# Kernel optimization log

Hardware: AMD Instinct MI355X
Metric: run time of the kernel (lower is better)

## Reference

```python
import jax, jax.numpy as jnp
import numpy as np

B = 64            # number of graphs
NPG = 64          # nodes per graph (static; lengths are all equal here)
N = B * NPG       # total nodes = sum(lengths)
LT = 128          # max text tokens per node
LL = 32           # max labels per node
VOCAB = 50000
TOTAL_NUM = 100000
D = 256           # embedding_text == embedding_label == hidden_dimension
OUT = 1024


def setup_inputs() -> dict:
    key = jax.random.key(0)
    ks = jax.random.split(key, 12)
    return {
        "text_ids": jax.random.randint(ks[0], (N, LT), 0, VOCAB),
        "label_ids": jax.random.randint(ks[1], (N, LL), 0, TOTAL_NUM),
        "text_len": jax.random.randint(ks[2], (N,), 1, LT + 1),
        "label_len": jax.random.randint(ks[3], (N,), 1, LL + 1),
        "word_emb": jax.random.normal(ks[4], (VOCAB, D), jnp.float32) * 0.02,
        "label_emb": jax.random.normal(ks[5], (TOTAL_NUM, D), jnp.float32) * 0.02,
        "Wg_text": jax.random.normal(ks[6], (D, D), jnp.float32) * (1.0 / np.sqrt(D)),
        "Wg_label": jax.random.normal(ks[7], (D, D), jnp.float32) * (1.0 / np.sqrt(D)),
        "w_adap": jax.random.normal(ks[8], (2,), jnp.float32),
        "W1": jax.random.normal(ks[9], (D, D), jnp.float32) * (1.0 / np.sqrt(D)),
        "b1": jnp.zeros((D,), jnp.float32),
        "Wout": jax.random.normal(ks[10], (D, OUT), jnp.float32) * (1.0 / np.sqrt(D)),
        "bout": jnp.zeros((OUT,), jnp.float32),
    }


def _ragged_bag(table, ids, lens, mean):
    # gather rows then masked sum over the ragged axis (EmbeddingBag-style)
    L = ids.shape[1]
    mask = (jnp.arange(L)[None, :] < lens[:, None]).astype(table.dtype)  # [N, L]
    emb = table[ids]                                                     # [N, L, D]
    out = jnp.einsum("nld,nl->nd", emb, mask)
    if mean:
        out = out / lens[:, None].astype(table.dtype)
    return out


def reference(text_ids, label_ids, text_len, label_len, word_emb, label_emb,
              Wg_text, Wg_label, w_adap, W1, b1, Wout, bout):
    # fetchFeature: per-node ragged mean of word embeddings, ragged sum of label embeddings
    text_out = _ragged_bag(word_emb, text_ids, text_len, mean=True)    # [N, D]
    label_out = _ragged_bag(label_emb, label_ids, label_len, mean=False)  # [N, D]

    # weighted_GCN surrogate: per-type linear projection + relu, then per-graph mean readout
    h_t = jax.nn.relu(text_out @ Wg_text)   # [N, D]
    h_l = jax.nn.relu(label_out @ Wg_label)  # [N, D]
    seg = jnp.repeat(jnp.arange(B), NPG)     # graph id per node
    r_t = jax.ops.segment_sum(h_t, seg, num_segments=B) / NPG  # [B, D]
    r_l = jax.ops.segment_sum(h_l, seg, num_segments=B) / NPG  # [B, D]

    # adap: Linear(2,1,bias=False) over stacked (text,label), then MLLinear fusion
    fused = jnp.stack([r_t, r_l], axis=-1) @ w_adap  # [B, D]
    h = jax.nn.relu(fused @ W1 + b1)
    return h @ Wout + bout  # [B, OUT]
```

## Files before the change

### kernel.cpp

```cpp
#include <hip/hip_runtime.h>

#define NN      4096
#define BG      64
#define NPG_    64
#define LT_     128
#define LL_     32
#define D_      256
#define OUT_    1024

typedef __attribute__((ext_vector_type(8))) short bf16x8;
typedef __attribute__((ext_vector_type(4))) float f32x4;

__device__ __forceinline__ void split_bf16(float v, unsigned short& hi, unsigned short& lo) {
    union { float f; unsigned u; } a; a.f = v;
    const unsigned hu = (a.u + 0x8000u) & 0xFFFF0000u;
    union { unsigned u; float f; } h; h.u = hu;
    const float r = v - h.f;
    union { float f; unsigned u; } b; b.f = r;
    hi = (unsigned short)(hu >> 16);
    lo = (unsigned short)(((b.u + 0x8000u) & 0xFFFF0000u) >> 16);
}

__global__ __launch_bounds__(256) void gather_kernel(
    const int*   __restrict__ text_ids,
    const int*   __restrict__ label_ids,
    const int*   __restrict__ text_len,
    const int*   __restrict__ label_len,
    const float* __restrict__ word_emb,
    const float* __restrict__ label_emb,
    const float* __restrict__ Wg_text,
    const float* __restrict__ Wg_label,
    unsigned short* __restrict__ Wpk,
    unsigned short* __restrict__ xh_t,
    unsigned short* __restrict__ xl_t,
    unsigned short* __restrict__ xh_l,
    unsigned short* __restrict__ xl_l)
{
    const int tid  = threadIdx.x;

    if (blockIdx.x >= NN) {
        const int b   = blockIdx.x - NN;
        const int mat = b >> 7;
        const int nt  = (b >> 3) & 15;
        const int ks  = b & 7;
        const float* __restrict__ W = mat ? Wg_label : Wg_text;
        #pragma unroll
        for (int r = 0; r < 2; ++r) {
            const int idx = tid + 256 * r;
            const int kl  = idx >> 4;
            const int c16 = idx & 15;
            const int k   = ks * 32 + kl;
            const float v = W[(size_t)k * D_ + nt * 16 + c16];
            unsigned short h, l;
            split_bf16(v, h, l);
            const int lane = c16 + 16 * ((kl >> 3) & 3);
            const int e    = kl & 7;
            const size_t pb = (((size_t)nt * 8 + ks) * 4 + mat * 2) * 512 + lane * 8 + e;
            Wpk[pb]       = h;
            Wpk[pb + 512] = l;
        }
        return;
    }

    __shared__ int   sIds[LT_ + LL_];
    __shared__ float redT[4][D_];
    __shared__ float redL[4][D_];

    const int n    = blockIdx.x;
    const int wave = tid >> 6;
    const int lane = tid & 63;

    if (tid < LT_)               sIds[tid] = text_ids [(size_t)n * LT_ + tid];
    else if (tid < LT_ + LL_)    sIds[tid] = label_ids[(size_t)n * LL_ + (tid - LT_)];
    const int lt = text_len[n];
    const int ll = label_len[n];
    __syncthreads();

    float4 aT = make_float4(0.f, 0.f, 0.f, 0.f);
    float4 aL = make_float4(0.f, 0.f, 0.f, 0.f);

    {
        const float* __restrict__ bp = word_emb + (size_t)lane * 4;
        #pragma unroll 8
        for (int l = wave; l < lt; l += 4) {
            const float4 v = *reinterpret_cast<const float4*>(bp + (size_t)sIds[l] * D_);
            aT.x += v.x; aT.y += v.y; aT.z += v.z; aT.w += v.w;
        }
    }
    {
        const float* __restrict__ bp = label_emb + (size_t)lane * 4;
        #pragma unroll 8
        for (int l = wave; l < ll; l += 4) {
            const float4 v = *reinterpret_cast<const float4*>(bp + (size_t)sIds[LT_ + l] * D_);
            aL.x += v.x; aL.y += v.y; aL.z += v.z; aL.w += v.w;
        }
    }

    *reinterpret_cast<float4*>(&redT[wave][lane * 4]) = aT;
    *reinterpret_cast<float4*>(&redL[wave][lane * 4]) = aL;
    __syncthreads();

    const float t  = ((redT[0][tid] + redT[1][tid]) + (redT[2][tid] + redT[3][tid])) / (float)lt;
    const float lv =  (redL[0][tid] + redL[1][tid]) + (redL[2][tid] + redL[3][tid]);

    unsigned short h, l;
    const size_t o = (size_t)n * D_ + tid;
    split_bf16(t,  h, l);  xh_t[o] = h;  xl_t[o] = l;
    split_bf16(lv, h, l);  xh_l[o] = h;  xl_l[o] = l;
}

__global__ __launch_bounds__(256, 4) void proj_kernel(
    const unsigned short* __restrict__ xh_t,
    const unsigned short* __restrict__ xl_t,
    const unsigned short* __restrict__ xh_l,
    const unsigned short* __restrict__ xl_l,
    const unsigned short* __restrict__ Wpk,
    const float* __restrict__ w_adap,
    float*       __restrict__ h_comb)
{
    __shared__ __align__(16) short ldsX[4][16 * D_];

    const int tid   = threadIdx.x;
    const int wave  = tid >> 6;
    const int lane  = tid & 63;
    const int ntile = blockIdx.x >> 2;
    const int cq    = blockIdx.x & 3;
    const int base  = ntile * 16;

    #pragma unroll
    for (int r = 0; r < 2; ++r) {
        const int idx = tid + 256 * r;
        const int nd  = idx >> 5, ch = idx & 31;
        const size_t g = (size_t)(base + nd) * D_ + ch * 8;
        const int d = nd * D_ + ((ch ^ (nd & 7)) * 8);
        *reinterpret_cast<int4*>(&ldsX[0][d]) = *reinterpret_cast<const int4*>(&xh_t[g]);
        *reinterpret_cast<int4*>(&ldsX[1][d]) = *reinterpret_cast<const int4*>(&xl_t[g]);
        *reinterpret_cast<int4*>(&ldsX[2][d]) = *reinterpret_cast<const int4*>(&xh_l[g]);
        *reinterpret_cast<int4*>(&ldsX[3][d]) = *reinterpret_cast<const int4*>(&xl_l[g]);
    }
    __syncthreads();

    const int nt  = cq * 4 + wave;
    const int row = lane & 15;
    const int kc  = lane >> 4;
    const unsigned short* __restrict__ WpB = Wpk + ((size_t)nt * 8) * 4 * 512 + lane * 8;

    f32x4 accT = {0.f, 0.f, 0.f, 0.f};
    f32x4 accL = {0.f, 0.f, 0.f, 0.f};

    bf16x8 cA0, cA1, cA2, cA3, cB0, cB1, cB2, cB3;
    bf16x8 nA0, nA1, nA2, nA3, nB0, nB1, nB2, nB3;

    {
        const int aidx = row * D_ + ((kc ^ (row & 7)) * 8);
        cA0 = *reinterpret_cast<const bf16x8*>(&ldsX[0][aidx]);
        cA1 = *reinterpret_cast<const bf16x8*>(&ldsX[1][aidx]);
        cA2 = *reinterpret_cast<const bf16x8*>(&ldsX[2][aidx]);
        cA3 = *reinterpret_cast<const bf16x8*>(&ldsX[3][aidx]);
        const unsigned short* p = WpB;
        cB0 = *reinterpret_cast<const bf16x8*>(p);
        cB1 = *reinterpret_cast<const bf16x8*>(p + 512);
        cB2 = *reinterpret_cast<const bf16x8*>(p + 1024);
        cB3 = *reinterpret_cast<const bf16x8*>(p + 1536);
    }

    #pragma unroll
    for (int ks = 0; ks < 8; ++ks) {
        if (ks < 7) {
            const int aidx = row * D_ + ((((ks + 1) * 4 + kc) ^ (row & 7)) * 8);
            nA0 = *reinterpret_cast<const bf16x8*>(&ldsX[0][aidx]);
            nA1 = *reinterpret_cast<const bf16x8*>(&ldsX[1][aidx]);
            nA2 = *reinterpret_cast<const bf16x8*>(&ldsX[2][aidx]);
            nA3 = *reinterpret_cast<const bf16x8*>(&ldsX[3][aidx]);
            const unsigned short* p = WpB + (size_t)(ks + 1) * 2048;
            nB0 = *reinterpret_cast<const bf16x8*>(p);
            nB1 = *reinterpret_cast<const bf16x8*>(p + 512);
            nB2 = *reinterpret_cast<const bf16x8*>(p + 1024);
            nB3 = *reinterpret_cast<const bf16x8*>(p + 1536);
        }

        accT = __builtin_amdgcn_mfma_f32_16x16x32_bf16(cA0, cB0, accT, 0, 0, 0);
        accT = __builtin_amdgcn_mfma_f32_16x16x32_bf16(cA0, cB1, accT, 0, 0, 0);
        accT = __builtin_amdgcn_mfma_f32_16x16x32_bf16(cA1, cB0, accT, 0, 0, 0);
        accL = __builtin_amdgcn_mfma_f32_16x16x32_bf16(cA2, cB2, accL, 0, 0, 0);
        accL = __builtin_amdgcn_mfma_f32_16x16x32_bf16(cA2, cB3, accL, 0, 0, 0);
        accL = __builtin_amdgcn_mfma_f32_16x16x32_bf16(cA3, cB2, accL, 0, 0, 0);

        cA0 = nA0; cA1 = nA1; cA2 = nA2; cA3 = nA3;
        cB0 = nB0; cB1 = nB1; cB2 = nB2; cB3 = nB3;
    }

    const float w0r = w_adap[0] * (1.0f / (float)NPG_);
    const float w1r = w_adap[1] * (1.0f / (float)NPG_);
    #pragma unroll
    for (int r = 0; r < 4; ++r) {
        const int node = base + kc * 4 + r;
        const int col  = nt * 16 + row;
        const float ht = accT[r] > 0.f ? accT[r] : 0.f;
        const float hl = accL[r] > 0.f ? accL[r] : 0.f;
        h_comb[(size_t)node * D_ + col] = w0r * ht + w1r * hl;
    }
}

__global__ __launch_bounds__(256) void graph_kernel(
    const float* __restrict__ h_comb,
    const float* __restrict__ W1,
    const float* __restrict__ b1,
    const float* __restrict__ Wout,
    const float* __restrict__ bout,
    float*       __restrict__ out)
{
    __shared__ float fused[D_];
    __shared__ float hrow[D_];

    const int bx   = blockIdx.x;
    const int b    = bx >> 2;
    const int part = bx & 3;
    const int tid  = threadIdx.x;

    float acc = 0.f;
    const float* __restrict__ basep = h_comb + (size_t)b * NPG_ * D_ + tid;
    #pragma unroll 8
    for (int n = 0; n < NPG_; ++n) acc += basep[(size_t)n * D_];
    fused[tid] = acc;
    __syncthreads();

    {
        float s0 = 0.f, s1 = 0.f, s2 = 0.f, s3 = 0.f;
        const float* __restrict__ wp = W1 + tid;
        for (int d = 0; d < D_; d += 4) {
            s0 = fmaf(fused[d + 0], wp[(size_t)(d + 0) * D_], s0);
            s1 = fmaf(fused[d + 1], wp[(size_t)(d + 1) * D_], s1);
            s2 = fmaf(fused[d + 2], wp[(size_t)(d + 2) * D_], s2);
            s3 = fmaf(fused[d + 3], wp[(size_t)(d + 3) * D_], s3);
        }
        const float a1 = b1[tid] + ((s0 + s1) + (s2 + s3));
        hrow[tid] = a1 > 0.f ? a1 : 0.f;
    }
    __syncthreads();

    const int j = part * 256 + tid;
    {
        float s0 = 0.f, s1 = 0.f, s2 = 0.f, s3 = 0.f;
        const float* __restrict__ wp = Wout + j;
        for (int d = 0; d < D_; d += 4) {
            s0 = fmaf(hrow[d + 0], wp[(size_t)(d + 0) * OUT_], s0);
            s1 = fmaf(hrow[d + 1], wp[(size_t)(d + 1) * OUT_], s1);
            s2 = fmaf(hrow[d + 2], wp[(size_t)(d + 2) * OUT_], s2);
            s3 = fmaf(hrow[d + 3], wp[(size_t)(d + 3) * OUT_], s3);
        }
        out[(size_t)b * OUT_ + j] = bout[j] + ((s0 + s1) + (s2 + s3));
    }
}

extern "C" void kernel_launch(void* const* d_in, const int* in_sizes, int n_in,
                              void* d_out, int out_size, void* d_ws, size_t ws_size,
                              hipStream_t stream) {
    const int*   text_ids  = (const int*)  d_in[0];
    const int*   label_ids = (const int*)  d_in[1];
    const int*   text_len  = (const int*)  d_in[2];
    const int*   label_len = (const int*)  d_in[3];
    const float* word_emb  = (const float*)d_in[4];
    const float* label_emb = (const float*)d_in[5];
    const float* Wg_text   = (const float*)d_in[6];
    const float* Wg_label  = (const float*)d_in[7];
    const float* w_adap    = (const float*)d_in[8];
    const float* W1        = (const float*)d_in[9];
    const float* b1        = (const float*)d_in[10];
    const float* Wout      = (const float*)d_in[11];
    const float* bout      = (const float*)d_in[12];

    char* ws = (char*)d_ws;
    float*          h_comb = (float*)ws;
    unsigned short* xh_t   = (unsigned short*)(ws + (4  << 20));
    unsigned short* xl_t   = (unsigned short*)(ws + (6  << 20));
    unsigned short* xh_l   = (unsigned short*)(ws + (8  << 20));
    unsigned short* xl_l   = (unsigned short*)(ws + (10 << 20));
    unsigned short* Wpk    = (unsigned short*)(ws + (12 << 20));
    float*          out    = (float*)d_out;

    gather_kernel<<<NN + 256, 256, 0, stream>>>(
        text_ids, label_ids, text_len, label_len,
        word_emb, label_emb, Wg_text, Wg_label, Wpk,
        xh_t, xl_t, xh_l, xl_l);

    proj_kernel<<<NN / 16 * 4, 256, 0, stream>>>(
        xh_t, xl_t, xh_l, xl_l, Wpk, w_adap, h_comb);

    graph_kernel<<<BG * 4, 256, 0, stream>>>(
        h_comb, W1, b1, Wout, bout, out);
}
```

Baseline: 84.70 us.

## Convert word table to bf16 each call and drop split-bf16 activation precision

Adds a prep kernel that converts the whole 50000x256 fp32 word embedding table to bf16 on every call, and gathers text rows from that half-size table. The gathered activations are now stored as single bf16 instead of a hi/lo split, which halves the workspace traffic and cuts the MFMA count in the projection from six to four per k-step. The cost is a full-table conversion pass (about 51MB read and 26MB written) on every call, plus lower precision in the activations and the embedding values.

```diff
diff --git a/kernel.cpp b/kernel.cpp
--- a/kernel.cpp
+++ b/kernel.cpp
@@ -7,10 +7,20 @@
 #define LL_     32
 #define D_      256
 #define OUT_    1024
+#define VOCAB_  50000
 
 typedef __attribute__((ext_vector_type(8))) short bf16x8;
 typedef __attribute__((ext_vector_type(4))) float f32x4;
 
+__device__ __forceinline__ unsigned short f2bf_rne(float f) {
+    union { float f; unsigned u; } a; a.f = f;
+    const unsigned r = a.u + 0x7FFFu + ((a.u >> 16) & 1u);
+    return (unsigned short)(r >> 16);
+}
+__device__ __forceinline__ float bf2f(unsigned short h) {
+    union { unsigned u; float f; } a; a.u = ((unsigned)h) << 16;
+    return a.f;
+}
 __device__ __forceinline__ void split_bf16(float v, unsigned short& hi, unsigned short& lo) {
     union { float f; unsigned u; } a; a.f = v;
     const unsigned hu = (a.u + 0x8000u) & 0xFFFF0000u;
@@ -21,52 +31,66 @@
     lo = (unsigned short)(((b.u + 0x8000u) & 0xFFFF0000u) >> 16);
 }
 
+__global__ __launch_bounds__(256) void prep_kernel(
+    const float* __restrict__ word_emb,
+    const float* __restrict__ Wg_text,
+    const float* __restrict__ Wg_label,
+    const int convBlocks,
+    unsigned short* __restrict__ wtab,
+    unsigned short* __restrict__ Wpk)
+{
+    const int tid = threadIdx.x;
+    if (blockIdx.x < convBlocks) {
+        const int total4 = VOCAB_ * D_ / 4;
+        const int stride = convBlocks * 256;
+        for (int i = blockIdx.x * 256 + tid; i < total4; i += stride) {
+            const float4 v = *reinterpret_cast<const float4*>(word_emb + (size_t)i * 4);
+            ushort4 o;
+            o.x = f2bf_rne(v.x); o.y = f2bf_rne(v.y);
+            o.z = f2bf_rne(v.z); o.w = f2bf_rne(v.w);
+            *reinterpret_cast<ushort4*>(wtab + (size_t)i * 4) = o;
+        }
+        return;
+    }
+    const int b   = blockIdx.x - convBlocks;
+    const int mat = b >> 7;
+    const int nt  = (b >> 3) & 15;
+    const int ks  = b & 7;
+    const float* __restrict__ W = mat ? Wg_label : Wg_text;
+    #pragma unroll
+    for (int r = 0; r < 2; ++r) {
+        const int idx = tid + 256 * r;
+        const int kl  = idx >> 4;
+        const int c16 = idx & 15;
+        const int k   = ks * 32 + kl;
+        const float v = W[(size_t)k * D_ + nt * 16 + c16];
+        unsigned short h, l;
+        split_bf16(v, h, l);
+        const int lane = c16 + 16 * ((kl >> 3) & 3);
+        const int e    = kl & 7;
+        const size_t pb = (((size_t)nt * 8 + ks) * 4 + mat * 2) * 512 + lane * 8 + e;
+        Wpk[pb]       = h;
+        Wpk[pb + 512] = l;
+    }
+}
+
+template<bool BF16TAB>
 __global__ __launch_bounds__(256) void gather_kernel(
     const int*   __restrict__ text_ids,
     const int*   __restrict__ label_ids,
     const int*   __restrict__ text_len,
     const int*   __restrict__ label_len,
     const float* __restrict__ word_emb,
+    const unsigned short* __restrict__ wtab,
     const float* __restrict__ label_emb,
-    const float* __restrict__ Wg_text,
-    const float* __restrict__ Wg_label,
-    unsigned short* __restrict__ Wpk,
-    unsigned short* __restrict__ xh_t,
-    unsigned short* __restrict__ xl_t,
-    unsigned short* __restrict__ xh_l,
-    unsigned short* __restrict__ xl_l)
+    unsigned short* __restrict__ xb_t,
+    unsigned short* __restrict__ xb_l)
 {
+    __shared__ int   sIds[LT_ + LL_];
+    __shared__ float red[8][D_];
+
+    const int n    = blockIdx.x;
     const int tid  = threadIdx.x;
-
-    if (blockIdx.x >= NN) {
-        const int b   = blockIdx.x - NN;
-        const int mat = b >> 7;
-        const int nt  = (b >> 3) & 15;
-        const int ks  = b & 7;
-        const float* __restrict__ W = mat ? Wg_label : Wg_text;
-        #pragma unroll
-        for (int r = 0; r < 2; ++r) {
-            const int idx = tid + 256 * r;
-            const int kl  = idx >> 4;
-            const int c16 = idx & 15;
-            const int k   = ks * 32 + kl;
-            const float v = W[(size_t)k * D_ + nt * 16 + c16];
-            unsigned short h, l;
-            split_bf16(v, h, l);
-            const int lane = c16 + 16 * ((kl >> 3) & 3);
-            const int e    = kl & 7;
-            const size_t pb = (((size_t)nt * 8 + ks) * 4 + mat * 2) * 512 + lane * 8 + e;
-            Wpk[pb]       = h;
-            Wpk[pb + 512] = l;
-        }
-        return;
-    }
-
-    __shared__ int   sIds[LT_ + LL_];
-    __shared__ float redT[4][D_];
-    __shared__ float redL[4][D_];
-
-    const int n    = blockIdx.x;
     const int wave = tid >> 6;
     const int lane = tid & 63;
 
@@ -76,17 +100,31 @@
     const int ll = label_len[n];
     __syncthreads();
 
-    float4 aT = make_float4(0.f, 0.f, 0.f, 0.f);
-    float4 aL = make_float4(0.f, 0.f, 0.f, 0.f);
-
-    {
+    float ta[8];
+    float4 aT4 = make_float4(0.f, 0.f, 0.f, 0.f);
+    if (BF16TAB) {
+        #pragma unroll
+        for (int j = 0; j < 8; ++j) ta[j] = 0.f;
+        const int h  = lane >> 5;
+        const int cg = lane & 31;
+        const int s  = wave * 2 + h;
+        const unsigned short* __restrict__ bp = wtab + cg * 8;
+        #pragma unroll 4
+        for (int l = s; l < lt; l += 8) {
+            const bf16x8 v = *reinterpret_cast<const bf16x8*>(bp + (size_t)sIds[l] * D_);
+            #pragma unroll
+            for (int j = 0; j < 8; ++j) ta[j] += bf2f((unsigned short)v[j]);
+        }
+    } else {
         const float* __restrict__ bp = word_emb + (size_t)lane * 4;
         #pragma unroll 8
         for (int l = wave; l < lt; l += 4) {
             const float4 v = *reinterpret_cast<const float4*>(bp + (size_t)sIds[l] * D_);
-            aT.x += v.x; aT.y += v.y; aT.z += v.z; aT.w += v.w;
-        }
-    }
+            aT4.x += v.x; aT4.y += v.y; aT4.z += v.z; aT4.w += v.w;
+        }
+    }
+
+    float4 aL = make_float4(0.f, 0.f, 0.f, 0.f);
     {
         const float* __restrict__ bp = label_emb + (size_t)lane * 4;
         #pragma unroll 8
@@ -96,29 +134,39 @@
         }
     }
 
-    *reinterpret_cast<float4*>(&redT[wave][lane * 4]) = aT;
-    *reinterpret_cast<float4*>(&redL[wave][lane * 4]) = aL;
-    __syncthreads();
-
-    const float t  = ((redT[0][tid] + redT[1][tid]) + (redT[2][tid] + redT[3][tid])) / (float)lt;
-    const float lv =  (redL[0][tid] + redL[1][tid]) + (redL[2][tid] + redL[3][tid]);
-
-    unsigned short h, l;
+    if (BF16TAB) {
+        const int h = lane >> 5, cg = lane & 31, s = wave * 2 + h;
+        *reinterpret_cast<float4*>(&red[s][cg * 8])     = make_float4(ta[0], ta[1], ta[2], ta[3]);
+        *reinterpret_cast<float4*>(&red[s][cg * 8 + 4]) = make_float4(ta[4], ta[5], ta[6], ta[7]);
+    } else {
+        *reinterpret_cast<float4*>(&red[wave][lane * 4]) = aT4;
+    }
+    __syncthreads();
+    float t;
+    if (BF16TAB)
+        t = ((red[0][tid] + red[1][tid]) + (red[2][tid] + red[3][tid]))
+          + ((red[4][tid] + red[5][tid]) + (red[6][tid] + red[7][tid]));
+    else
+        t = (red[0][tid] + red[1][tid]) + (red[2][tid] + red[3][tid]);
+    t /= (float)lt;
     const size_t o = (size_t)n * D_ + tid;
-    split_bf16(t,  h, l);  xh_t[o] = h;  xl_t[o] = l;
-    split_bf16(lv, h, l);  xh_l[o] = h;  xl_l[o] = l;
+    xb_t[o] = f2bf_rne(t);
+    __syncthreads();
+
+    *reinterpret_cast<float4*>(&red[wave][lane * 4]) = aL;
+    __syncthreads();
+    const float lv = (red[0][tid] + red[1][tid]) + (red[2][tid] + red[3][tid]);
+    xb_l[o] = f2bf_rne(lv);
 }
 
 __global__ __launch_bounds__(256, 4) void proj_kernel(
-    const unsigned short* __restrict__ xh_t,
-    const unsigned short* __restrict__ xl_t,
-    const unsigned short* __restrict__ xh_l,
-    const unsigned short* __restrict__ xl_l,
+    const unsigned short* __restrict__ xb_t,
+    const unsigned short* __restrict__ xb_l,
     const unsigned short* __restrict__ Wpk,
     const float* __restrict__ w_adap,
     float*       __restrict__ h_comb)
 {
-    __shared__ __align__(16) short ldsX[4][16 * D_];
+    __shared__ __align__(16) short ldsX[2][16 * D_];
 
     const int tid   = threadIdx.x;
     const int wave  = tid >> 6;
@@ -133,10 +181,8 @@
         const int nd  = idx >> 5, ch = idx & 31;
         const size_t g = (size_t)(base + nd) * D_ + ch * 8;
         const int d = nd * D_ + ((ch ^ (nd & 7)) * 8);
-        *reinterpret_cast<int4*>(&ldsX[0][d]) = *reinterpret_cast<const int4*>(&xh_t[g]);
-        *reinterpret_cast<int4*>(&ldsX[1][d]) = *reinterpret_cast<const int4*>(&xl_t[g]);
-        *reinterpret_cast<int4*>(&ldsX[2][d]) = *reinterpret_cast<const int4*>(&xh_l[g]);
-        *reinterpret_cast<int4*>(&ldsX[3][d]) = *reinterpret_cast<const int4*>(&xl_l[g]);
+        *reinterpret_cast<int4*>(&ldsX[0][d]) = *reinterpret_cast<const int4*>(&xb_t[g]);
+        *reinterpret_cast<int4*>(&ldsX[1][d]) = *reinterpret_cast<const int4*>(&xb_l[g]);
     }
     __syncthreads();
 
@@ -148,15 +194,13 @@
     f32x4 accT = {0.f, 0.f, 0.f, 0.f};
     f32x4 accL = {0.f, 0.f, 0.f, 0.f};
 
-    bf16x8 cA0, cA1, cA2, cA3, cB0, cB1, cB2, cB3;
-    bf16x8 nA0, nA1, nA2, nA3, nB0, nB1, nB2, nB3;
+    bf16x8 cA0, cA1, cB0, cB1, cB2, cB3;
+    bf16x8 nA0, nA1, nB0, nB1, nB2, nB3;
 
     {
         const int aidx = row * D_ + ((kc ^ (row & 7)) * 8);
         cA0 = *reinterpret_cast<const bf16x8*>(&ldsX[0][aidx]);
         cA1 = *reinterpret_cast<const bf16x8*>(&ldsX[1][aidx]);
-        cA2 = *reinterpret_cast<const bf16x8*>(&ldsX[2][aidx]);
-        cA3 = *reinterpret_cast<const bf16x8*>(&ldsX[3][aidx]);
         const unsigned short* p = WpB;
         cB0 = *reinterpret_cast<const bf16x8*>(p);
         cB1 = *reinterpret_cast<const bf16x8*>(p + 512);
@@ -170,8 +214,6 @@
             const int aidx = row * D_ + ((((ks + 1) * 4 + kc) ^ (row & 7)) * 8);
             nA0 = *reinterpret_cast<const bf16x8*>(&ldsX[0][aidx]);
             nA1 = *reinterpret_cast<const bf16x8*>(&ldsX[1][aidx]);
-            nA2 = *reinterpret_cast<const bf16x8*>(&ldsX[2][aidx]);
-            nA3 = *reinterpret_cast<const bf16x8*>(&ldsX[3][aidx]);
             const unsigned short* p = WpB + (size_t)(ks + 1) * 2048;
             nB0 = *reinterpret_cast<const bf16x8*>(p);
             nB1 = *reinterpret_cast<const bf16x8*>(p + 512);
@@ -181,12 +223,10 @@
 
         accT = __builtin_amdgcn_mfma_f32_16x16x32_bf16(cA0, cB0, accT, 0, 0, 0);
         accT = __builtin_amdgcn_mfma_f32_16x16x32_bf16(cA0, cB1, accT, 0, 0, 0);
-        accT = __builtin_amdgcn_mfma_f32_16x16x32_bf16(cA1, cB0, accT, 0, 0, 0);
-        accL = __builtin_amdgcn_mfma_f32_16x16x32_bf16(cA2, cB2, accL, 0, 0, 0);
-        accL = __builtin_amdgcn_mfma_f32_16x16x32_bf16(cA2, cB3, accL, 0, 0, 0);
-        accL = __builtin_amdgcn_mfma_f32_16x16x32_bf16(cA3, cB2, accL, 0, 0, 0);
-
-        cA0 = nA0; cA1 = nA1; cA2 = nA2; cA3 = nA3;
+        accL = __builtin_amdgcn_mfma_f32_16x16x32_bf16(cA1, cB2, accL, 0, 0, 0);
+        accL = __builtin_amdgcn_mfma_f32_16x16x32_bf16(cA1, cB3, accL, 0, 0, 0);
+
+        cA0 = nA0; cA1 = nA1;
         cB0 = nB0; cB1 = nB1; cB2 = nB2; cB3 = nB3;
     }
 
@@ -272,20 +312,31 @@
 
     char* ws = (char*)d_ws;
     float*          h_comb = (float*)ws;
-    unsigned short* xh_t   = (unsigned short*)(ws + (4  << 20));
-    unsigned short* xl_t   = (unsigned short*)(ws + (6  << 20));
-    unsigned short* xh_l   = (unsigned short*)(ws + (8  << 20));
-    unsigned short* xl_l   = (unsigned short*)(ws + (10 << 20));
-    unsigned short* Wpk    = (unsigned short*)(ws + (12 << 20));
+    unsigned short* xb_t   = (unsigned short*)(ws + (4 << 20));
+    unsigned short* xb_l   = (unsigned short*)(ws + (6 << 20));
+    unsigned short* Wpk    = (unsigned short*)(ws + (8 << 20));
+    unsigned short* wtab   = (unsigned short*)(ws + (9 << 20));
     float*          out    = (float*)d_out;
 
-    gather_kernel<<<NN + 256, 256, 0, stream>>>(
-        text_ids, label_ids, text_len, label_len,
-        word_emb, label_emb, Wg_text, Wg_label, Wpk,
-        xh_t, xl_t, xh_l, xl_l);
+    const size_t need = (size_t)(9 << 20) + (size_t)VOCAB_ * D_ * 2;
+    const bool useBf16 = ws_size >= need;
+    const int convBlocks = useBf16 ? 2048 : 0;
+
+    prep_kernel<<<convBlocks + 256, 256, 0, stream>>>(
+        word_emb, Wg_text, Wg_label, convBlocks, wtab, Wpk);
+
+    if (useBf16) {
+        gather_kernel<true><<<NN, 256, 0, stream>>>(
+            text_ids, label_ids, text_len, label_len,
+            word_emb, wtab, label_emb, xb_t, xb_l);
+    } else {
+        gather_kernel<false><<<NN, 256, 0, stream>>>(
+            text_ids, label_ids, text_len, label_len,
+            word_emb, wtab, label_emb, xb_t, xb_l);
+    }
 
     proj_kernel<<<NN / 16 * 4, 256, 0, stream>>>(
-        xh_t, xl_t, xh_l, xl_l, Wpk, w_adap, h_comb);
+        xb_t, xb_l, Wpk, w_adap, h_comb);
 
     graph_kernel<<<BG * 4, 256, 0, stream>>>(
         h_comb, W1, b1, Wout, bout, out);
```

Measured after the change: 75.41 us. 1.12x faster.
